# Kernel tuning notes

Hardware: AMD Instinct MI355X
Metric: run time of the kernel (lower is better)

The kernel has to match this reference:

```python
import jax, jax.numpy as jnp
import numpy as np

B, C, N = 2, 64, 40000
MLP = [64, 64, 128]
EPS = 1e-5


def setup_inputs() -> dict:
    key = jax.random.key(0)
    ks = jax.random.split(key, 2 + 4 * len(MLP))
    inp = {
        "points": jax.random.normal(ks[0], (B, C, N), dtype=jnp.float32),
        "near_idx": jax.random.randint(ks[1], (N, 6), 0, 2 * N, dtype=jnp.int32),
    }
    last = 2 * C
    for i, out_ch in enumerate(MLP):
        k = 2 + 4 * i
        scale = 1.0 / np.sqrt(last)
        inp[f"W{i}"] = jax.random.normal(ks[k], (out_ch, last), dtype=jnp.float32) * scale
        inp[f"b{i}"] = jax.random.normal(ks[k + 1], (out_ch,), dtype=jnp.float32) * 0.01
        inp[f"g{i}"] = jnp.ones((out_ch,), dtype=jnp.float32)
        inp[f"beta{i}"] = jnp.zeros((out_ch,), dtype=jnp.float32)
        last = out_ch
    return inp


def _mlp_bn_relu(x, W, b, g, beta):
    # x: [B, N, 6, Cin]; 1x1 conv == channel matmul
    y = jnp.einsum("bnkc,oc->bnko", x, W) + b
    mu = y.mean(axis=(0, 1, 2))
    var = y.var(axis=(0, 1, 2))  # biased, matches BN training normalization
    y = (y - mu) * jax.lax.rsqrt(var + EPS) * g + beta
    return jax.nn.relu(y)


def reference(points, near_idx, W0, b0, g0, beta0, W1, b1, g1, beta1, W2, b2, g2, beta2):
    x = jnp.transpose(points, (0, 2, 1))          # [B, N, C]
    pad = jnp.full_like(x, -1.0)                  # out-of-index block (-1 fill)
    xpad = jnp.concatenate([x, pad], axis=1)      # [B, 2N, C]
    near = xpad[:, near_idx, :]                   # [B, N, 6, C] irregular gather
    feat = jnp.concatenate(
        [jnp.broadcast_to(x[:, :, None, :], near.shape), near], axis=3
    )                                             # [B, N, 6, 2C]
    feat = _mlp_bn_relu(feat, W0, b0, g0, beta0)
    feat = _mlp_bn_relu(feat, W1, b1, g1, beta1)
    feat = _mlp_bn_relu(feat, W2, b2, g2, beta2)  # [B, N, 6, C']
    new_feature = feat.max(axis=2)                # max over 6 neighbors -> [B, N, C']
    new_feature = jnp.transpose(new_feature, (0, 2, 1))  # [B, C', N] (torch layout)
    out_feature = new_feature.max(axis=1)         # max over channels -> [B, N]
    return (out_feature, new_feature)
```

## Files before the change

kernel.cpp:

```cpp
#include <hip/hip_runtime.h>

typedef unsigned short u16;
typedef unsigned int uint;
typedef short bf16x8 __attribute__((ext_vector_type(8)));
typedef float f32x4 __attribute__((ext_vector_type(4)));

constexpr int B_ = 2;
constexpr int N_ = 40000;
constexpr int SPB = 240000;
constexpr int S_ = B_ * SPB;
constexpr float EPS_ = 1e-5f;
constexpr float INV_S = 1.0f / (float)S_;
constexpr int OF_ = B_ * N_;
constexpr int TILES_PB = SPB / 48;

constexpr int      WS_V_U16   = B_ * N_ * 128;
constexpr size_t   NEED_BIG_B = 81955072ull;

__device__ inline float b2f_lo(uint u) { return __builtin_bit_cast(float, u << 16); }
__device__ inline float b2f_hi(uint u) { return __builtin_bit_cast(float, u & 0xffff0000u); }
__device__ inline float b2fu(u16 s)    { return __builtin_bit_cast(float, ((uint)s) << 16); }
__device__ inline u16 f2b(float f) {
    uint b = __builtin_bit_cast(uint, f);
    return (u16)((b + 0x7fffu + ((b >> 16) & 1u)) >> 16);
}
__device__ inline uint pk2(float a, float b) { return (uint)f2b(a) | ((uint)f2b(b) << 16); }
__device__ inline void unp8(uint4 q, float* f) {
    f[0] = b2f_lo(q.x); f[1] = b2f_hi(q.x); f[2] = b2f_lo(q.y); f[3] = b2f_hi(q.y);
    f[4] = b2f_lo(q.z); f[5] = b2f_hi(q.z); f[6] = b2f_lo(q.w); f[7] = b2f_hi(q.w);
}

__global__ __launch_bounds__(256) void wprep_kernel(const float* __restrict__ W0,
                                                    const float* __restrict__ W1,
                                                    const float* __restrict__ W2,
                                                    float* __restrict__ stats,
                                                    float* __restrict__ neg2,
                                                    u16* __restrict__ pack) {
    const int t = threadIdx.x;
    stats[t] = 0.f; stats[t + 256] = 0.f;
    if (t < 64) {
        float s = 0.f;
        for (int j = 0; j < 64; ++j) s += W0[t * 128 + 64 + j];
        neg2[t] = -s;
    }
    for (int g = t; g < 40 * 64; g += 256) {
        int lane = g & 63, grp = g >> 6;
        int cb = lane & 15, kq = lane >> 4;
        ushort4 lo, hi;
        u16* dst;
        if (grp < 16) {
            int ct = grp >> 1, kk = grp & 1;
            int c = ct * 16 + cb, jb = kk * 32 + kq * 8;
            dst = pack + g * 8;
            float v[8];
            #pragma unroll
            for (int i = 0; i < 8; ++i)
                v[i] = (c < 64) ? W0[c * 128 + jb + i] : W0[(c - 64) * 128 + 64 + jb + i];
            lo = {f2b(v[0]), f2b(v[1]), f2b(v[2]), f2b(v[3])};
            hi = {f2b(v[4]), f2b(v[5]), f2b(v[6]), f2b(v[7])};
        } else if (grp < 24) {
            int g2 = grp - 16;
            int ct = g2 >> 1, kk = g2 & 1;
            const float* wp = W1 + (ct * 16 + cb) * 64 + kk * 32 + kq * 8;
            dst = pack + 8192 + (g2 * 64 + lane) * 8;
            lo = {f2b(wp[0]), f2b(wp[1]), f2b(wp[2]), f2b(wp[3])};
            hi = {f2b(wp[4]), f2b(wp[5]), f2b(wp[6]), f2b(wp[7])};
        } else {
            int g3 = grp - 24;
            int ct = g3 >> 1, kk = g3 & 1;
            const float* wp = W2 + (ct * 16 + cb) * 64 + kk * 32 + kq * 8;
            dst = pack + 12288 + (g3 * 64 + lane) * 8;
            lo = {f2b(wp[0]), f2b(wp[1]), f2b(wp[2]), f2b(wp[3])};
            hi = {f2b(wp[4]), f2b(wp[5]), f2b(wp[6]), f2b(wp[7])};
        }
        *(ushort4*)dst = lo;
        *(ushort4*)(dst + 4) = hi;
    }
}

__global__ __launch_bounds__(256) void p0_kernel(const float* __restrict__ pts,
                                                 const u16* __restrict__ pack,
                                                 u16* __restrict__ V) {
    const int t = threadIdx.x, lane = t & 63, w = t >> 6;
    const int cb = lane & 15, kq = lane >> 4;
    const int b = blockIdx.y;
    const int n0 = blockIdx.x * 192 + w * 48;
    const uint4* mp = (const uint4*)pack;

    bf16x8 af[3][2];
    #pragma unroll
    for (int mt = 0; mt < 3; ++mt) {
        int n = n0 + mt * 16 + cb;
        int nc = (n < N_) ? n : (N_ - 1);
        const float* xp = pts + b * 64 * N_ + nc;
        #pragma unroll
        for (int kk = 0; kk < 2; ++kk) {
            int jb = kk * 32 + kq * 8;
            #pragma unroll
            for (int i = 0; i < 8; ++i)
                af[mt][kk][i] = (short)f2b(xp[(size_t)(jb + i) * N_]);
        }
    }
    #pragma unroll
    for (int ct = 0; ct < 8; ++ct) {
        bf16x8 b0 = __builtin_bit_cast(bf16x8, mp[(ct * 2 + 0) * 64 + lane]);
        bf16x8 b1 = __builtin_bit_cast(bf16x8, mp[(ct * 2 + 1) * 64 + lane]);
        #pragma unroll
        for (int mt = 0; mt < 3; ++mt) {
            f32x4 acc = {};
            acc = __builtin_amdgcn_mfma_f32_16x16x32_bf16(af[mt][0], b0, acc, 0, 0, 0);
            acc = __builtin_amdgcn_mfma_f32_16x16x32_bf16(af[mt][1], b1, acc, 0, 0, 0);
            int rbase = n0 + mt * 16 + kq * 4;
            #pragma unroll
            for (int r = 0; r < 4; ++r) {
                int n = rbase + r;
                if (n < N_) V[(size_t)(b * N_ + n) * 128 + ct * 16 + cb] = f2b(acc[r]);
            }
        }
    }
}

__global__ __launch_bounds__(256) void p1_kernel(const u16* __restrict__ V,
                                                 const int* __restrict__ nidx,
                                                 const float* __restrict__ neg2,
                                                 float* __restrict__ stats) {
    const int t = threadIdx.x, lane = t & 63, w = t >> 6;
    const int slot = lane >> 3, cg = lane & 7;
    const int b = blockIdx.y;
    const int s0 = blockIdx.x * 384 + w * 96;
    float ngs8[8];
    #pragma unroll
    for (int i = 0; i < 8; ++i) ngs8[i] = neg2[cg * 8 + i];
    float sum[8] = {0,0,0,0,0,0,0,0}, sq[8] = {0,0,0,0,0,0,0,0};
    #pragma unroll
    for (int h = 0; h < 2; ++h) {
        int mh[6]; uint4 q1[6], q2[6]; bool val[6];
        #pragma unroll
        for (int it = 0; it < 6; ++it) {
            int s = s0 + (h * 6 + it) * 8 + slot;
            mh[it] = nidx[s];
            q1[it] = *(const uint4*)(V + (size_t)(b * N_ + s / 6) * 128 + cg * 8);
        }
        #pragma unroll
        for (int it = 0; it < 6; ++it) {
            val[it] = (mh[it] < N_);
            int row2 = val[it] ? (b * N_ + mh[it]) : 0;
            q2[it] = *(const uint4*)(V + (size_t)row2 * 128 + 64 + cg * 8);
        }
        #pragma unroll
        for (int it = 0; it < 6; ++it) {
            float v1[8], v2[8];
            unp8(q1[it], v1); unp8(q2[it], v2);
            #pragma unroll
            for (int i = 0; i < 8; ++i) {
                float z = v1[i] + (val[it] ? v2[i] : ngs8[i]);
                sum[i] += z; sq[i] = fmaf(z, z, sq[i]);
            }
        }
    }
    #pragma unroll
    for (int i = 0; i < 8; ++i) {
        sum[i] += __shfl_xor(sum[i], 8); sum[i] += __shfl_xor(sum[i], 16); sum[i] += __shfl_xor(sum[i], 32);
        sq[i]  += __shfl_xor(sq[i], 8);  sq[i]  += __shfl_xor(sq[i], 16);  sq[i]  += __shfl_xor(sq[i], 32);
    }
    __shared__ float red[2][4][64];
    if (slot == 0) {
        #pragma unroll
        for (int i = 0; i < 8; ++i) { red[0][w][cg * 8 + i] = sum[i]; red[1][w][cg * 8 + i] = sq[i]; }
    }
    __syncthreads();
    if (t < 64) {
        float s_ = (red[0][0][t] + red[0][1][t]) + (red[0][2][t] + red[0][3][t]);
        float q_ = (red[1][0][t] + red[1][1][t]) + (red[1][2][t] + red[1][3][t]);
        atomicAdd(&stats[t], s_);
        atomicAdd(&stats[64 + t], q_);
    }
}

__device__ inline bf16x8 build_af(const u16* __restrict__ V, int row1, int row2,
                                  const float* adt0, const float* adt1,
                                  const float* ngs, int j0) {
    float v1f[8], v2f[8];
    uint4 q1 = *(const uint4*)(V + (size_t)row1 * 128 + j0);
    unp8(q1, v1f);
    if (row2 >= 0) {
        uint4 q2 = *(const uint4*)(V + (size_t)row2 * 128 + 64 + j0);
        unp8(q2, v2f);
    } else {
        #pragma unroll
        for (int i = 0; i < 8; ++i) v2f[i] = ngs[j0 + i];
    }
    bf16x8 r;
    #pragma unroll
    for (int i = 0; i < 8; ++i) {
        float f0 = fmaxf((v1f[i] + v2f[i]) * adt0[j0 + i] + adt1[j0 + i], 0.f);
        r[i] = (short)f2b(f0);
    }
    return r;
}

__device__ inline int sigma_sl(int mt, int row) {
    int r_ = row & 3, kqr = row >> 2;
    int idx = mt * 4 + r_;
    int po = (idx >= 6) ? 1 : 0;
    return (kqr * 2 + po) * 6 + (idx - 6 * po);
}

template<int STOREZ1>
__global__ __launch_bounds__(256) void p2_kernel(const u16* __restrict__ V,
                                                 const int* __restrict__ nidx,
                                                 const float* __restrict__ neg2,
                                                 const u16* __restrict__ pack,
                                                 const float* __restrict__ g0,
                                                 const float* __restrict__ beta0,
                                                 float* __restrict__ stats,
                                                 u16* __restrict__ z1buf) {
    __shared__ float adt0[64], adt1[64], ngs[64];
    __shared__ float red[2][4][64];
    const int t = threadIdx.x, lane = t & 63, w = t >> 6;
    const int cb = lane & 15, kq = lane >> 4;
    if (t < 64) {
        float mu = stats[t] * INV_S, vr = stats[64 + t] * INV_S - mu * mu;
        float a = rsqrtf(vr + EPS_) * g0[t];
        adt0[t] = a; adt1[t] = beta0[t] - mu * a; ngs[t] = neg2[t];
    }
    __syncthreads();
    const int b = blockIdx.y;
    const int slb = blockIdx.x * 192 + w * 48;
    const uint4* w1p = (const uint4*)(pack + 8192);
    uint4* zt4 = STOREZ1 ? ((uint4*)z1buf + ((size_t)b * TILES_PB + blockIdx.x * 4 + w) * (6 * 64)) : nullptr;

    int m_[3];
    #pragma unroll
    for (int mt = 0; mt < 3; ++mt) m_[mt] = nidx[slb + sigma_sl(mt, cb)];

    bf16x8 bf[4][2];
    #pragma unroll
    for (int ct = 0; ct < 4; ++ct)
        #pragma unroll
        for (int kk = 0; kk < 2; ++kk)
            bf[ct][kk] = __builtin_bit_cast(bf16x8, w1p[(ct * 2 + kk) * 64 + lane]);

    float ssum[4] = {0,0,0,0}, ssq[4] = {0,0,0,0};
    #pragma unroll
    for (int mt = 0; mt < 3; ++mt) {
        int sl = slb + sigma_sl(mt, cb);
        int n = sl / 6;
        int row1 = b * N_ + n;
        int row2 = (m_[mt] < N_) ? (b * N_ + m_[mt]) : -1;
        bf16x8 af[2];
        #pragma unroll
        for (int kk = 0; kk < 2; ++kk)
            af[kk] = build_af(V, row1, row2, adt0, adt1, ngs, kk * 32 + kq * 8);
        f32x4 acc[4] = {};
        #pragma unroll
        for (int ct = 0; ct < 4; ++ct) {
            acc[ct] = __builtin_amdgcn_mfma_f32_16x16x32_bf16(af[0], bf[ct][0], acc[ct], 0, 0, 0);
            acc[ct] = __builtin_amdgcn_mfma_f32_16x16x32_bf16(af[1], bf[ct][1], acc[ct], 0, 0, 0);
        }
        #pragma unroll
        for (int ct = 0; ct < 4; ++ct)
            #pragma unroll
            for (int r = 0; r < 4; ++r) {
                float z = acc[ct][r];
                ssum[ct] += z; ssq[ct] = fmaf(z, z, ssq[ct]);
            }
        if constexpr (STOREZ1) {
            #pragma unroll
            for (int cp = 0; cp < 2; ++cp) {
                uint4 o;
                o.x = pk2(acc[cp * 2][0], acc[cp * 2][1]);
                o.y = pk2(acc[cp * 2][2], acc[cp * 2][3]);
                o.z = pk2(acc[cp * 2 + 1][0], acc[cp * 2 + 1][1]);
                o.w = pk2(acc[cp * 2 + 1][2], acc[cp * 2 + 1][3]);
                zt4[(mt * 2 + cp) * 64 + lane] = o;
            }
        }
    }
    #pragma unroll
    for (int ct = 0; ct < 4; ++ct) {
        ssum[ct] += __shfl_xor(ssum[ct], 16); ssum[ct] += __shfl_xor(ssum[ct], 32);
        ssq[ct]  += __shfl_xor(ssq[ct], 16);  ssq[ct]  += __shfl_xor(ssq[ct], 32);
    }
    if (lane < 16) {
        #pragma unroll
        for (int ct = 0; ct < 4; ++ct) {
            red[0][w][ct * 16 + lane] = ssum[ct];
            red[1][w][ct * 16 + lane] = ssq[ct];
        }
    }
    __syncthreads();
    if (t < 64) {
        float s = (red[0][0][t] + red[0][1][t]) + (red[0][2][t] + red[0][3][t]);
        float q = (red[1][0][t] + red[1][1][t]) + (red[1][2][t] + red[1][3][t]);
        atomicAdd(&stats[128 + t], s);
        atomicAdd(&stats[192 + t], q);
    }
}

__global__ __launch_bounds__(256) void p3big_kernel(const u16* __restrict__ z1buf,
                                                    const u16* __restrict__ pack,
                                                    const float* __restrict__ g1, const float* __restrict__ beta1,
                                                    const float* __restrict__ g2,
                                                    float* __restrict__ stats,
                                                    u16* __restrict__ raw) {
    __shared__ u16   f1t[4][2][1024];
    __shared__ float smax[32][129];
    __shared__ float red[2][4][128];
    __shared__ float adt2s[64], adt3s[64], psign[128];
    const int t = threadIdx.x, lane = t & 63, w = t >> 6;
    const int cb = lane & 15, kq = lane >> 4;
    if (t < 64) {
        float mu1 = stats[128 + t] * INV_S, vr1 = stats[192 + t] * INV_S - mu1 * mu1;
        float a1 = rsqrtf(vr1 + EPS_) * g1[t];
        adt2s[t] = a1; adt3s[t] = beta1[t] - mu1 * a1;
    }
    if (t < 128) psign[t] = (g2[t] >= 0.f) ? 1.f : -1.f;
    __syncthreads();

    const int b = blockIdx.y;
    const uint4* zt4 = (const uint4*)z1buf + ((size_t)b * TILES_PB + blockIdx.x * 4 + w) * (6 * 64);
    const uint4* w2p = (const uint4*)(pack + 12288);

    uint4 zq[6];
    #pragma unroll
    for (int i = 0; i < 6; ++i) zq[i] = zt4[i * 64 + lane];

    bf16x8 bf2[8][2];
    #pragma unroll
    for (int u = 0; u < 8; ++u)
        #pragma unroll
        for (int kk = 0; kk < 2; ++kk)
            bf2[u][kk] = __builtin_bit_cast(bf16x8, w2p[(u * 2 + kk) * 64 + lane]);

    float a1c[4], d1c[4];
    #pragma unroll
    for (int ct = 0; ct < 4; ++ct) { a1c[ct] = adt2s[ct * 16 + cb]; d1c[ct] = adt3s[ct * 16 + cb]; }

    float pmax_[2][4][2];
    #pragma unroll
    for (int h = 0; h < 2; ++h)
        #pragma unroll
        for (int ct = 0; ct < 4; ++ct) { pmax_[h][ct][0] = -3.402823466e+38f; pmax_[h][ct][1] = -3.402823466e+38f; }
    float ssum[8] = {0,0,0,0,0,0,0,0}, ssq[8] = {0,0,0,0,0,0,0,0};
    u16* fb0 = f1t[w][0];
    u16* fb1 = f1t[w][1];

    auto BNW = [&](int mt, u16* fb) {
        #pragma unroll
        for (int cp = 0; cp < 2; ++cp) {
            uint4 q = zq[mt * 2 + cp];
            float za[4] = {b2f_lo(q.x), b2f_hi(q.x), b2f_lo(q.y), b2f_hi(q.y)};
            float zb[4] = {b2f_lo(q.z), b2f_hi(q.z), b2f_lo(q.w), b2f_hi(q.w)};
            int ca = cp * 2, cc = cp * 2 + 1;
            #pragma unroll
            for (int r = 0; r < 4; ++r) {
                int rw = kq * 4 + r;
                fb[rw * 64 + ((ca * 16 + cb) ^ ((rw & 7) << 3))] = f2b(fmaxf(za[r] * a1c[ca] + d1c[ca], 0.f));
                fb[rw * 64 + ((cc * 16 + cb) ^ ((rw & 7) << 3))] = f2b(fmaxf(zb[r] * a1c[cc] + d1c[cc], 0.f));
            }
        }
    };
    auto RDA = [&](const u16* fb, bf16x8* af2) {
        #pragma unroll
        for (int kk = 0; kk < 2; ++kk) {
            int j0 = kk * 32 + kq * 8;
            af2[kk] = __builtin_bit_cast(bf16x8, *(const uint4*)(fb + cb * 64 + (j0 ^ ((cb & 7) << 3))));
        }
    };
    auto MM = [&](int mt, const bf16x8* af2) {
        #pragma unroll
        for (int half = 0; half < 2; ++half) {
            f32x4 acc2[4] = {};
            #pragma unroll
            for (int ct = 0; ct < 4; ++ct) {
                acc2[ct] = __builtin_amdgcn_mfma_f32_16x16x32_bf16(af2[0], bf2[half * 4 + ct][0], acc2[ct], 0, 0, 0);
                acc2[ct] = __builtin_amdgcn_mfma_f32_16x16x32_bf16(af2[1], bf2[half * 4 + ct][1], acc2[ct], 0, 0, 0);
            }
            #pragma unroll
            for (int ct = 0; ct < 4; ++ct) {
                float ps = psign[half * 64 + ct * 16 + cb];
                #pragma unroll
                for (int r = 0; r < 4; ++r) {
                    float z = acc2[ct][r];
                    ssum[half * 4 + ct] += z;
                    ssq[half * 4 + ct] = fmaf(z, z, ssq[half * 4 + ct]);
                    float zz = z * ps;
                    int pi = (mt == 0) ? 0 : ((mt == 2) ? 1 : ((r >= 2) ? 1 : 0));
                    pmax_[half][ct][pi] = fmaxf(pmax_[half][ct][pi], zz);
                }
            }
        }
    };

    bf16x8 afA[2], afB[2];
    BNW(0, fb0); BNW(1, fb1);
    RDA(fb0, afA);
    MM(0, afA);
    BNW(2, fb0);
    RDA(fb1, afB);
    MM(1, afB);
    RDA(fb0, afA);
    MM(2, afA);

    #pragma unroll
    for (int half = 0; half < 2; ++half)
        #pragma unroll
        for (int ct = 0; ct < 4; ++ct)
            #pragma unroll
            for (int p = 0; p < 2; ++p)
                smax[w * 8 + kq * 2 + p][half * 64 + ct * 16 + cb] = pmax_[half][ct][p];
    #pragma unroll
    for (int j = 0; j < 8; ++j) {
        ssum[j] += __shfl_xor(ssum[j], 16); ssum[j] += __shfl_xor(ssum[j], 32);
        ssq[j]  += __shfl_xor(ssq[j], 16);  ssq[j]  += __shfl_xor(ssq[j], 32);
    }
    if (lane < 16) {
        #pragma unroll
        for (int j = 0; j < 8; ++j) {
            int c = (j >> 2) * 64 + (j & 3) * 16 + lane;
            red[0][w][c] = ssum[j];
            red[1][w][c] = ssq[j];
        }
    }
    __syncthreads();
    if (t < 128) {
        float s = (red[0][0][t] + red[0][1][t]) + (red[0][2][t] + red[0][3][t]);
        float q = (red[1][0][t] + red[1][1][t]) + (red[1][2][t] + red[1][3][t]);
        atomicAdd(&stats[256 + t], s);
        atomicAdd(&stats[384 + t], q);
    }
    {
        int c2 = t >> 1, nh = t & 1;
        float ps = psign[c2];
        u16* rp = raw + ((size_t)b * 128 + c2) * N_ + blockIdx.x * 32 + nh * 16;
        #pragma unroll
        for (int i4 = 0; i4 < 4; ++i4) {
            ushort4 v;
            v.x = f2b(smax[nh * 16 + i4 * 4 + 0][c2] * ps);
            v.y = f2b(smax[nh * 16 + i4 * 4 + 1][c2] * ps);
            v.z = f2b(smax[nh * 16 + i4 * 4 + 2][c2] * ps);
            v.w = f2b(smax[nh * 16 + i4 * 4 + 3][c2] * ps);
            *(ushort4*)(rp + i4 * 4) = v;
        }
    }
}

__global__ __launch_bounds__(256) void p3small_kernel(const u16* __restrict__ V,
                                                      const int* __restrict__ nidx,
                                                      const float* __restrict__ neg2,
                                                      const u16* __restrict__ pack,
                                                      const float* __restrict__ g0, const float* __restrict__ beta0,
                                                      const float* __restrict__ g1, const float* __restrict__ beta1,
                                                      const float* __restrict__ g2,
                                                      float* __restrict__ stats,
                                                      float* __restrict__ out) {
    __shared__ u16   f1t[4][16 * 64];
    __shared__ float smax[32][129];
    __shared__ float red[2][4][128];
    __shared__ float adt2s[64], adt3s[64], psign[128];
    __shared__ float adt0s[64], adt1s[64], ngs[64];
    const int t = threadIdx.x, lane = t & 63, w = t >> 6;
    const int cb = lane & 15, kq = lane >> 4;
    if (t < 64) {
        float mu1 = stats[128 + t] * INV_S, vr1 = stats[192 + t] * INV_S - mu1 * mu1;
        float a1 = rsqrtf(vr1 + EPS_) * g1[t];
        adt2s[t] = a1; adt3s[t] = beta1[t] - mu1 * a1;
        float mu0 = stats[t] * INV_S, vr0 = stats[64 + t] * INV_S - mu0 * mu0;
        float a0 = rsqrtf(vr0 + EPS_) * g0[t];
        adt0s[t] = a0; adt1s[t] = beta0[t] - mu0 * a0; ngs[t] = neg2[t];
    }
    if (t < 128) psign[t] = (g2[t] >= 0.f) ? 1.f : -1.f;
    __syncthreads();

    const int b = blockIdx.y;
    const int slb = blockIdx.x * 192 + w * 48;
    const uint4* w1p = (const uint4*)(pack + 8192);
    const uint4* w2p = (const uint4*)(pack + 12288);

    bf16x8 bf2[8][2];
    #pragma unroll
    for (int u = 0; u < 8; ++u)
        #pragma unroll
        for (int kk = 0; kk < 2; ++kk)
            bf2[u][kk] = __builtin_bit_cast(bf16x8, w2p[(u * 2 + kk) * 64 + lane]);

    float a1c[4], d1c[4];
    #pragma unroll
    for (int ct = 0; ct < 4; ++ct) { a1c[ct] = adt2s[ct * 16 + cb]; d1c[ct] = adt3s[ct * 16 + cb]; }

    float pmax_[2][4][2];
    #pragma unroll
    for (int h = 0; h < 2; ++h)
        #pragma unroll
        for (int ct = 0; ct < 4; ++ct) { pmax_[h][ct][0] = -3.402823466e+38f; pmax_[h][ct][1] = -3.402823466e+38f; }
    float ssum[8] = {0,0,0,0,0,0,0,0}, ssq[8] = {0,0,0,0,0,0,0,0};
    u16* fb = f1t[w];

    #pragma unroll
    for (int mt = 0; mt < 3; ++mt) {
        bf16x8 bf1[4][2];
        #pragma unroll
        for (int ct = 0; ct < 4; ++ct)
            #pragma unroll
            for (int kk = 0; kk < 2; ++kk)
                bf1[ct][kk] = __builtin_bit_cast(bf16x8, w1p[(ct * 2 + kk) * 64 + lane]);
        int sl = slb + sigma_sl(mt, cb);
        int n = sl / 6;
        int m = nidx[sl];
        int row1 = b * N_ + n;
        int row2 = (m < N_) ? (b * N_ + m) : -1;
        bf16x8 af[2];
        #pragma unroll
        for (int kk = 0; kk < 2; ++kk)
            af[kk] = build_af(V, row1, row2, adt0s, adt1s, ngs, kk * 32 + kq * 8);
        f32x4 z1v[4];
        #pragma unroll
        for (int ct = 0; ct < 4; ++ct) {
            f32x4 a = {};
            a = __builtin_amdgcn_mfma_f32_16x16x32_bf16(af[0], bf1[ct][0], a, 0, 0, 0);
            a = __builtin_amdgcn_mfma_f32_16x16x32_bf16(af[1], bf1[ct][1], a, 0, 0, 0);
            z1v[ct] = a;
        }
        #pragma unroll
        for (int ct = 0; ct < 4; ++ct)
            #pragma unroll
            for (int r = 0; r < 4; ++r) {
                float f1 = fmaxf(z1v[ct][r] * a1c[ct] + d1c[ct], 0.f);
                int rw = kq * 4 + r;
                fb[rw * 64 + ((ct * 16 + cb) ^ ((rw & 7) << 3))] = f2b(f1);
            }
        bf16x8 af2[2];
        #pragma unroll
        for (int kk = 0; kk < 2; ++kk) {
            int j0 = kk * 32 + kq * 8;
            af2[kk] = __builtin_bit_cast(bf16x8, *(const uint4*)(fb + cb * 64 + (j0 ^ ((cb & 7) << 3))));
        }
        #pragma unroll
        for (int half = 0; half < 2; ++half) {
            f32x4 acc2[4] = {};
            #pragma unroll
            for (int ct = 0; ct < 4; ++ct) {
                acc2[ct] = __builtin_amdgcn_mfma_f32_16x16x32_bf16(af2[0], bf2[half * 4 + ct][0], acc2[ct], 0, 0, 0);
                acc2[ct] = __builtin_amdgcn_mfma_f32_16x16x32_bf16(af2[1], bf2[half * 4 + ct][1], acc2[ct], 0, 0, 0);
            }
            #pragma unroll
            for (int ct = 0; ct < 4; ++ct) {
                float ps = psign[half * 64 + ct * 16 + cb];
                #pragma unroll
                for (int r = 0; r < 4; ++r) {
                    float z = acc2[ct][r];
                    ssum[half * 4 + ct] += z;
                    ssq[half * 4 + ct] = fmaf(z, z, ssq[half * 4 + ct]);
                    float zz = z * ps;
                    int pi = (mt == 0) ? 0 : ((mt == 2) ? 1 : ((r >= 2) ? 1 : 0));
                    pmax_[half][ct][pi] = fmaxf(pmax_[half][ct][pi], zz);
                }
            }
        }
    }
    #pragma unroll
    for (int half = 0; half < 2; ++half)
        #pragma unroll
        for (int ct = 0; ct < 4; ++ct)
            #pragma unroll
            for (int p = 0; p < 2; ++p)
                smax[w * 8 + kq * 2 + p][half * 64 + ct * 16 + cb] = pmax_[half][ct][p];
    #pragma unroll
    for (int j = 0; j < 8; ++j) {
        ssum[j] += __shfl_xor(ssum[j], 16); ssum[j] += __shfl_xor(ssum[j], 32);
        ssq[j]  += __shfl_xor(ssq[j], 16);  ssq[j]  += __shfl_xor(ssq[j], 32);
    }
    if (lane < 16) {
        #pragma unroll
        for (int j = 0; j < 8; ++j) {
            int c = (j >> 2) * 64 + (j & 3) * 16 + lane;
            red[0][w][c] = ssum[j];
            red[1][w][c] = ssq[j];
        }
    }
    __syncthreads();
    if (t < 128) {
        float s = (red[0][0][t] + red[0][1][t]) + (red[0][2][t] + red[0][3][t]);
        float q = (red[1][0][t] + red[1][1][t]) + (red[1][2][t] + red[1][3][t]);
        atomicAdd(&stats[256 + t], s);
        atomicAdd(&stats[384 + t], q);
    }
    {
        int c2 = t >> 1, nh = t & 1;
        float ps = psign[c2];
        float* op = out + OF_ + ((size_t)b * 128 + c2) * N_ + blockIdx.x * 32 + nh * 16;
        #pragma unroll
        for (int i4 = 0; i4 < 4; ++i4) {
            float4 v;
            v.x = smax[nh * 16 + i4 * 4 + 0][c2] * ps;
            v.y = smax[nh * 16 + i4 * 4 + 1][c2] * ps;
            v.z = smax[nh * 16 + i4 * 4 + 2][c2] * ps;
            v.w = smax[nh * 16 + i4 * 4 + 3][c2] * ps;
            *(float4*)(op + i4 * 4) = v;
        }
    }
}

__global__ __launch_bounds__(256) void p4big_kernel(const float* __restrict__ g2,
                                                    const float* __restrict__ beta2,
                                                    const float* __restrict__ stats,
                                                    const u16* __restrict__ raw,
                                                    float* __restrict__ out) {
    __shared__ float a2s[128], d2s[128];
    __shared__ float vred[4][64];
    const int t = threadIdx.x, lane = t & 63, cg = t >> 6;
    if (t < 128) {
        float mu = stats[256 + t] * INV_S;
        float vr = stats[384 + t] * INV_S - mu * mu;
        float a = rsqrtf(vr + EPS_) * g2[t];
        a2s[t] = a;
        d2s[t] = beta2[t] - mu * a;
    }
    __syncthreads();
    const int b = blockIdx.y;
    const int n = blockIdx.x * 64 + lane;
    const u16* rp = raw + ((size_t)b * 128 + cg * 32) * N_ + n;
    float* op = out + OF_ + ((size_t)b * 128 + cg * 32) * N_ + n;
    float vmax = -3.402823466e+38f;
    #pragma unroll 8
    for (int c = 0; c < 32; ++c) {
        int c2 = cg * 32 + c;
        float v = fmaxf(b2fu(rp[(size_t)c * N_]) * a2s[c2] + d2s[c2], 0.f);
        op[(size_t)c * N_] = v;
        vmax = fmaxf(vmax, v);
    }
    vred[cg][lane] = vmax;
    __syncthreads();
    if (t < 64)
        out[b * N_ + blockIdx.x * 64 + t] =
            fmaxf(fmaxf(vred[0][t], vred[1][t]), fmaxf(vred[2][t], vred[3][t]));
}

__global__ __launch_bounds__(256) void p4small_kernel(const float* __restrict__ g2,
                                                      const float* __restrict__ beta2,
                                                      const float* __restrict__ stats,
                                                      float* __restrict__ outbuf) {
    __shared__ float a2s[128], d2s[128];
    const int t = threadIdx.x;
    if (t < 128) {
        float mu = stats[256 + t] * INV_S;
        float vr = stats[384 + t] * INV_S - mu * mu;
        float a = rsqrtf(vr + EPS_) * g2[t];
        a2s[t] = a;
        d2s[t] = beta2[t] - mu * a;
    }
    __syncthreads();
    const int b = blockIdx.y;
    const int n = blockIdx.x * 256 + t;
    if (n >= N_) return;
    float vmax = -3.402823466e+38f;
    #pragma unroll 8
    for (int c2 = 0; c2 < 128; ++c2) {
        size_t idx = OF_ + ((size_t)b * 128 + c2) * N_ + n;
        float v = fmaxf(outbuf[idx] * a2s[c2] + d2s[c2], 0.f);
        outbuf[idx] = v;
        vmax = fmaxf(vmax, v);
    }
    outbuf[b * N_ + n] = vmax;
}

extern "C" void kernel_launch(void* const* d_in, const int* in_sizes, int n_in,
                              void* d_out, int out_size, void* d_ws, size_t ws_size,
                              hipStream_t stream) {
    (void)in_sizes; (void)n_in; (void)out_size;
    const float* pts   = (const float*)d_in[0];
    const int*   nidx  = (const int*)d_in[1];
    const float* W0    = (const float*)d_in[2];
    const float* g0    = (const float*)d_in[4];
    const float* beta0 = (const float*)d_in[5];
    const float* W1    = (const float*)d_in[6];
    const float* g1    = (const float*)d_in[8];
    const float* beta1 = (const float*)d_in[9];
    const float* W2    = (const float*)d_in[10];
    const float* g2    = (const float*)d_in[12];
    const float* beta2 = (const float*)d_in[13];
    const bool big = ws_size >= NEED_BIG_B;
    u16*   V     = (u16*)d_ws;
    u16*   z1b   = big ? ((u16*)d_ws + WS_V_U16) : nullptr;
    float* stats = (float*)d_ws + (big ? 20480000 : 5120000);
    float* neg2  = stats + 512;
    u16*   pack  = (u16*)d_ws + (big ? 40961152 : 10241152);
    float* out   = (float*)d_out;

    hipLaunchKernelGGL(wprep_kernel, dim3(1), dim3(256), 0, stream, W0, W1, W2, stats, neg2, pack);
    hipLaunchKernelGGL(p0_kernel, dim3((N_ + 191) / 192, B_), dim3(256), 0, stream, pts, pack, V);
    hipLaunchKernelGGL(p1_kernel, dim3(SPB / 384, B_), dim3(256), 0, stream, V, nidx, neg2, stats);
    if (big) {
        hipLaunchKernelGGL((p2_kernel<1>), dim3(SPB / 192, B_), dim3(256), 0, stream,
                           V, nidx, neg2, pack, g0, beta0, stats, z1b);
        hipLaunchKernelGGL(p3big_kernel, dim3(TILES_PB / 4, B_), dim3(256), 0, stream,
                           z1b, pack, g1, beta1, g2, stats, V);
        hipLaunchKernelGGL(p4big_kernel, dim3(N_ / 64, B_), dim3(256), 0, stream,
                           g2, beta2, stats, V, out);
    } else {
        hipLaunchKernelGGL((p2_kernel<0>), dim3(SPB / 192, B_), dim3(256), 0, stream,
                           V, nidx, neg2, pack, g0, beta0, stats, nullptr);
        hipLaunchKernelGGL(p3small_kernel, dim3(SPB / 192, B_), dim3(256), 0, stream,
                           V, nidx, neg2, pack, g0, beta0, g1, beta1, g2, stats, out);
        hipLaunchKernelGGL(p4small_kernel, dim3((N_ + 255) / 256, B_), dim3(256), 0, stream,
                           g2, beta2, stats, out);
    }
}
```

Measured before the change: 298.5 us.

## Materialize layer-0 pre-activations in p1 and recompute layer-1 in p3 instead of storing z1

```diff
diff --git a/kernel.cpp b/kernel.cpp
--- a/kernel.cpp
+++ b/kernel.cpp
@@ -12,7 +12,6 @@
 constexpr float EPS_ = 1e-5f;
 constexpr float INV_S = 1.0f / (float)S_;
 constexpr int OF_ = B_ * N_;
-constexpr int TILES_PB = SPB / 48;
 
 constexpr int      WS_V_U16   = B_ * N_ * 128;
 constexpr size_t   NEED_BIG_B = 81955072ull;
@@ -120,14 +119,17 @@
     }
 }
 
+template<int STOREZ0>
 __global__ __launch_bounds__(256) void p1_kernel(const u16* __restrict__ V,
                                                  const int* __restrict__ nidx,
                                                  const float* __restrict__ neg2,
-                                                 float* __restrict__ stats) {
+                                                 float* __restrict__ stats,
+                                                 u16* __restrict__ z0) {
     const int t = threadIdx.x, lane = t & 63, w = t >> 6;
     const int slot = lane >> 3, cg = lane & 7;
     const int b = blockIdx.y;
     const int s0 = blockIdx.x * 384 + w * 96;
+    uint4* zw = STOREZ0 ? ((uint4*)z0 + (size_t)b * SPB * 8) : nullptr;
     float ngs8[8];
     #pragma unroll
     for (int i = 0; i < 8; ++i) ngs8[i] = neg2[cg * 8 + i];
@@ -149,12 +151,17 @@
         }
         #pragma unroll
         for (int it = 0; it < 6; ++it) {
-            float v1[8], v2[8];
+            float v1[8], v2[8], z[8];
             unp8(q1[it], v1); unp8(q2[it], v2);
             #pragma unroll
             for (int i = 0; i < 8; ++i) {
-                float z = v1[i] + (val[it] ? v2[i] : ngs8[i]);
-                sum[i] += z; sq[i] = fmaf(z, z, sq[i]);
+                z[i] = v1[i] + (val[it] ? v2[i] : ngs8[i]);
+                sum[i] += z[i]; sq[i] = fmaf(z[i], z[i], sq[i]);
+            }
+            if constexpr (STOREZ0) {
+                int s = s0 + (h * 6 + it) * 8 + slot;
+                uint4 o = {pk2(z[0], z[1]), pk2(z[2], z[3]), pk2(z[4], z[5]), pk2(z[6], z[7])};
+                zw[(size_t)s * 8 + cg] = o;
             }
         }
     }
@@ -199,6 +206,19 @@
     return r;
 }
 
+__device__ inline void af_from_z0(uint4 q1, uint4 q2, int kq,
+                                  const float* adt0, const float* adt1, bf16x8* af) {
+    float z1[8], z2[8];
+    unp8(q1, z1); unp8(q2, z2);
+    bf16x8 a0, a1;
+    #pragma unroll
+    for (int i = 0; i < 8; ++i) {
+        a0[i] = (short)f2b(fmaxf(z1[i] * adt0[kq * 8 + i] + adt1[kq * 8 + i], 0.f));
+        a1[i] = (short)f2b(fmaxf(z2[i] * adt0[32 + kq * 8 + i] + adt1[32 + kq * 8 + i], 0.f));
+    }
+    af[0] = a0; af[1] = a1;
+}
+
 __device__ inline int sigma_sl(int mt, int row) {
     int r_ = row & 3, kqr = row >> 2;
     int idx = mt * 4 + r_;
@@ -206,34 +226,33 @@
     return (kqr * 2 + po) * 6 + (idx - 6 * po);
 }
 
-template<int STOREZ1>
-__global__ __launch_bounds__(256) void p2_kernel(const u16* __restrict__ V,
-                                                 const int* __restrict__ nidx,
-                                                 const float* __restrict__ neg2,
-                                                 const u16* __restrict__ pack,
-                                                 const float* __restrict__ g0,
-                                                 const float* __restrict__ beta0,
-                                                 float* __restrict__ stats,
-                                                 u16* __restrict__ z1buf) {
-    __shared__ float adt0[64], adt1[64], ngs[64];
+__global__ __launch_bounds__(256) void p2big_kernel(const u16* __restrict__ z0,
+                                                    const u16* __restrict__ pack,
+                                                    const float* __restrict__ g0,
+                                                    const float* __restrict__ beta0,
+                                                    float* __restrict__ stats) {
+    __shared__ float adt0[64], adt1[64];
     __shared__ float red[2][4][64];
     const int t = threadIdx.x, lane = t & 63, w = t >> 6;
     const int cb = lane & 15, kq = lane >> 4;
     if (t < 64) {
         float mu = stats[t] * INV_S, vr = stats[64 + t] * INV_S - mu * mu;
         float a = rsqrtf(vr + EPS_) * g0[t];
-        adt0[t] = a; adt1[t] = beta0[t] - mu * a; ngs[t] = neg2[t];
+        adt0[t] = a; adt1[t] = beta0[t] - mu * a;
     }
     __syncthreads();
     const int b = blockIdx.y;
     const int slb = blockIdx.x * 192 + w * 48;
+    const uint4* zr = (const uint4*)z0 + (size_t)(b * SPB + slb) * 8;
     const uint4* w1p = (const uint4*)(pack + 8192);
-    uint4* zt4 = STOREZ1 ? ((uint4*)z1buf + ((size_t)b * TILES_PB + blockIdx.x * 4 + w) * (6 * 64)) : nullptr;
-
-    int m_[3];
-    #pragma unroll
-    for (int mt = 0; mt < 3; ++mt) m_[mt] = nidx[slb + sigma_sl(mt, cb)];
-
+
+    uint4 zq[6];
+    #pragma unroll
+    for (int mt = 0; mt < 3; ++mt) {
+        int sig = sigma_sl(mt, cb);
+        zq[mt * 2 + 0] = zr[sig * 8 + kq];
+        zq[mt * 2 + 1] = zr[sig * 8 + 4 + kq];
+    }
     bf16x8 bf[4][2];
     #pragma unroll
     for (int ct = 0; ct < 4; ++ct)
@@ -244,14 +263,8 @@
     float ssum[4] = {0,0,0,0}, ssq[4] = {0,0,0,0};
     #pragma unroll
     for (int mt = 0; mt < 3; ++mt) {
-        int sl = slb + sigma_sl(mt, cb);
-        int n = sl / 6;
-        int row1 = b * N_ + n;
-        int row2 = (m_[mt] < N_) ? (b * N_ + m_[mt]) : -1;
         bf16x8 af[2];
-        #pragma unroll
-        for (int kk = 0; kk < 2; ++kk)
-            af[kk] = build_af(V, row1, row2, adt0, adt1, ngs, kk * 32 + kq * 8);
+        af_from_z0(zq[mt * 2], zq[mt * 2 + 1], kq, adt0, adt1, af);
         f32x4 acc[4] = {};
         #pragma unroll
         for (int ct = 0; ct < 4; ++ct) {
@@ -265,17 +278,6 @@
                 float z = acc[ct][r];
                 ssum[ct] += z; ssq[ct] = fmaf(z, z, ssq[ct]);
             }
-        if constexpr (STOREZ1) {
-            #pragma unroll
-            for (int cp = 0; cp < 2; ++cp) {
-                uint4 o;
-                o.x = pk2(acc[cp * 2][0], acc[cp * 2][1]);
-                o.y = pk2(acc[cp * 2][2], acc[cp * 2][3]);
-                o.z = pk2(acc[cp * 2 + 1][0], acc[cp * 2 + 1][1]);
-                o.w = pk2(acc[cp * 2 + 1][2], acc[cp * 2 + 1][3]);
-                zt4[(mt * 2 + cp) * 64 + lane] = o;
-            }
-        }
     }
     #pragma unroll
     for (int ct = 0; ct < 4; ++ct) {
@@ -298,19 +300,23 @@
     }
 }
 
-__global__ __launch_bounds__(256) void p3big_kernel(const u16* __restrict__ z1buf,
+__global__ __launch_bounds__(256) void p3big_kernel(const u16* __restrict__ z0,
                                                     const u16* __restrict__ pack,
+                                                    const float* __restrict__ g0, const float* __restrict__ beta0,
                                                     const float* __restrict__ g1, const float* __restrict__ beta1,
                                                     const float* __restrict__ g2,
                                                     float* __restrict__ stats,
                                                     u16* __restrict__ raw) {
-    __shared__ u16   f1t[4][2][1024];
+    __shared__ u16   f1t[4][1024];
     __shared__ float smax[32][129];
     __shared__ float red[2][4][128];
-    __shared__ float adt2s[64], adt3s[64], psign[128];
+    __shared__ float adt0s[64], adt1s[64], adt2s[64], adt3s[64], psign[128];
     const int t = threadIdx.x, lane = t & 63, w = t >> 6;
     const int cb = lane & 15, kq = lane >> 4;
     if (t < 64) {
+        float mu0 = stats[t] * INV_S, vr0 = stats[64 + t] * INV_S - mu0 * mu0;
+        float a0 = rsqrtf(vr0 + EPS_) * g0[t];
+        adt0s[t] = a0; adt1s[t] = beta0[t] - mu0 * a0;
         float mu1 = stats[128 + t] * INV_S, vr1 = stats[192 + t] * INV_S - mu1 * mu1;
         float a1 = rsqrtf(vr1 + EPS_) * g1[t];
         adt2s[t] = a1; adt3s[t] = beta1[t] - mu1 * a1;
@@ -319,13 +325,18 @@
     __syncthreads();
 
     const int b = blockIdx.y;
-    const uint4* zt4 = (const uint4*)z1buf + ((size_t)b * TILES_PB + blockIdx.x * 4 + w) * (6 * 64);
+    const int slb = blockIdx.x * 192 + w * 48;
+    const uint4* zr = (const uint4*)z0 + (size_t)(b * SPB + slb) * 8;
+    const uint4* w1p = (const uint4*)(pack + 8192);
     const uint4* w2p = (const uint4*)(pack + 12288);
 
     uint4 zq[6];
     #pragma unroll
-    for (int i = 0; i < 6; ++i) zq[i] = zt4[i * 64 + lane];
-
+    for (int mt = 0; mt < 3; ++mt) {
+        int sig = sigma_sl(mt, cb);
+        zq[mt * 2 + 0] = zr[sig * 8 + kq];
+        zq[mt * 2 + 1] = zr[sig * 8 + 4 + kq];
+    }
     bf16x8 bf2[8][2];
     #pragma unroll
     for (int u = 0; u < 8; ++u)
@@ -343,32 +354,40 @@
         #pragma unroll
         for (int ct = 0; ct < 4; ++ct) { pmax_[h][ct][0] = -3.402823466e+38f; pmax_[h][ct][1] = -3.402823466e+38f; }
     float ssum[8] = {0,0,0,0,0,0,0,0}, ssq[8] = {0,0,0,0,0,0,0,0};
-    u16* fb0 = f1t[w][0];
-    u16* fb1 = f1t[w][1];
-
-    auto BNW = [&](int mt, u16* fb) {
-        #pragma unroll
-        for (int cp = 0; cp < 2; ++cp) {
-            uint4 q = zq[mt * 2 + cp];
-            float za[4] = {b2f_lo(q.x), b2f_hi(q.x), b2f_lo(q.y), b2f_hi(q.y)};
-            float zb[4] = {b2f_lo(q.z), b2f_hi(q.z), b2f_lo(q.w), b2f_hi(q.w)};
-            int ca = cp * 2, cc = cp * 2 + 1;
+    u16* fb = f1t[w];
+
+    #pragma unroll
+    for (int mt = 0; mt < 3; ++mt) {
+        bf16x8 af[2];
+        af_from_z0(zq[mt * 2], zq[mt * 2 + 1], kq, adt0s, adt1s, af);
+        bf16x8 bf1[4][2];
+        #pragma unroll
+        for (int ct = 0; ct < 4; ++ct)
+            #pragma unroll
+            for (int kk = 0; kk < 2; ++kk)
+                bf1[ct][kk] = __builtin_bit_cast(bf16x8, w1p[(ct * 2 + kk) * 64 + lane]);
+        f32x4 z1v[4];
+        #pragma unroll
+        for (int ct = 0; ct < 4; ++ct) {
+            f32x4 a = {};
+            a = __builtin_amdgcn_mfma_f32_16x16x32_bf16(af[0], bf1[ct][0], a, 0, 0, 0);
+            a = __builtin_amdgcn_mfma_f32_16x16x32_bf16(af[1], bf1[ct][1], a, 0, 0, 0);
+            z1v[ct] = a;
+        }
+        #pragma unroll
+        for (int ct = 0; ct < 4; ++ct)
             #pragma unroll
             for (int r = 0; r < 4; ++r) {
+                float f1 = fmaxf(z1v[ct][r] * a1c[ct] + d1c[ct], 0.f);
                 int rw = kq * 4 + r;
-                fb[rw * 64 + ((ca * 16 + cb) ^ ((rw & 7) << 3))] = f2b(fmaxf(za[r] * a1c[ca] + d1c[ca], 0.f));
-                fb[rw * 64 + ((cc * 16 + cb) ^ ((rw & 7) << 3))] = f2b(fmaxf(zb[r] * a1c[cc] + d1c[cc], 0.f));
-            }
-        }
-    };
-    auto RDA = [&](const u16* fb, bf16x8* af2) {
+                fb[rw * 64 + ((ct * 16 + cb) ^ ((rw & 7) << 3))] = f2b(f1);
+            }
+        bf16x8 af2[2];
         #pragma unroll
         for (int kk = 0; kk < 2; ++kk) {
             int j0 = kk * 32 + kq * 8;
             af2[kk] = __builtin_bit_cast(bf16x8, *(const uint4*)(fb + cb * 64 + (j0 ^ ((cb & 7) << 3))));
         }
-    };
-    auto MM = [&](int mt, const bf16x8* af2) {
         #pragma unroll
         for (int half = 0; half < 2; ++half) {
             f32x4 acc2[4] = {};
@@ -391,18 +410,7 @@
                 }
             }
         }
-    };
-
-    bf16x8 afA[2], afB[2];
-    BNW(0, fb0); BNW(1, fb1);
-    RDA(fb0, afA);
-    MM(0, afA);
-    BNW(2, fb0);
-    RDA(fb1, afB);
-    MM(1, afB);
-    RDA(fb0, afA);
-    MM(2, afA);
-
+    }
     #pragma unroll
     for (int half = 0; half < 2; ++half)
         #pragma unroll
@@ -443,6 +451,79 @@
             v.w = f2b(smax[nh * 16 + i4 * 4 + 3][c2] * ps);
             *(ushort4*)(rp + i4 * 4) = v;
         }
+    }
+}
+
+__global__ __launch_bounds__(256) void p2small_kernel(const u16* __restrict__ V,
+                                                      const int* __restrict__ nidx,
+                                                      const float* __restrict__ neg2,
+                                                      const u16* __restrict__ pack,
+                                                      const float* __restrict__ g0,
+                                                      const float* __restrict__ beta0,
+                                                      float* __restrict__ stats) {
+    __shared__ float adt0[64], adt1[64], ngs[64];
+    __shared__ float red[2][4][64];
+    const int t = threadIdx.x, lane = t & 63, w = t >> 6;
+    const int cb = lane & 15, kq = lane >> 4;
+    if (t < 64) {
+        float mu = stats[t] * INV_S, vr = stats[64 + t] * INV_S - mu * mu;
+        float a = rsqrtf(vr + EPS_) * g0[t];
+        adt0[t] = a; adt1[t] = beta0[t] - mu * a; ngs[t] = neg2[t];
+    }
+    __syncthreads();
+    const int b = blockIdx.y;
+    const int slb = blockIdx.x * 192 + w * 48;
+    const uint4* w1p = (const uint4*)(pack + 8192);
+    bf16x8 bf[4][2];
+    #pragma unroll
+    for (int ct = 0; ct < 4; ++ct)
+        #pragma unroll
+        for (int kk = 0; kk < 2; ++kk)
+            bf[ct][kk] = __builtin_bit_cast(bf16x8, w1p[(ct * 2 + kk) * 64 + lane]);
+    float ssum[4] = {0,0,0,0}, ssq[4] = {0,0,0,0};
+    #pragma unroll
+    for (int mt = 0; mt < 3; ++mt) {
+        int sl = slb + sigma_sl(mt, cb);
+        int n = sl / 6;
+        int m = nidx[sl];
+        int row1 = b * N_ + n;
+        int row2 = (m < N_) ? (b * N_ + m) : -1;
+        bf16x8 af[2];
+        #pragma unroll
+        for (int kk = 0; kk < 2; ++kk)
+            af[kk] = build_af(V, row1, row2, adt0, adt1, ngs, kk * 32 + kq * 8);
+        f32x4 acc[4] = {};
+        #pragma unroll
+        for (int ct = 0; ct < 4; ++ct) {
+            acc[ct] = __builtin_amdgcn_mfma_f32_16x16x32_bf16(af[0], bf[ct][0], acc[ct], 0, 0, 0);
+            acc[ct] = __builtin_amdgcn_mfma_f32_16x16x32_bf16(af[1], bf[ct][1], acc[ct], 0, 0, 0);
+        }
+        #pragma unroll
+        for (int ct = 0; ct < 4; ++ct)
+            #pragma unroll
+            for (int r = 0; r < 4; ++r) {
+                float z = acc[ct][r];
+                ssum[ct] += z; ssq[ct] = fmaf(z, z, ssq[ct]);
+            }
+    }
+    #pragma unroll
+    for (int ct = 0; ct < 4; ++ct) {
+        ssum[ct] += __shfl_xor(ssum[ct], 16); ssum[ct] += __shfl_xor(ssum[ct], 32);
+        ssq[ct]  += __shfl_xor(ssq[ct], 16);  ssq[ct]  += __shfl_xor(ssq[ct], 32);
+    }
+    if (lane < 16) {
+        #pragma unroll
+        for (int ct = 0; ct < 4; ++ct) {
+            red[0][w][ct * 16 + lane] = ssum[ct];
+            red[1][w][ct * 16 + lane] = ssq[ct];
+        }
+    }
+    __syncthreads();
+    if (t < 64) {
+        float s = (red[0][0][t] + red[0][1][t]) + (red[0][2][t] + red[0][3][t]);
+        float q = (red[1][0][t] + red[1][1][t]) + (red[1][2][t] + red[1][3][t]);
+        atomicAdd(&stats[128 + t], s);
+        atomicAdd(&stats[192 + t], q);
     }
 }
 
@@ -455,7 +536,7 @@
                                                       const float* __restrict__ g2,
                                                       float* __restrict__ stats,
                                                       float* __restrict__ out) {
-    __shared__ u16   f1t[4][16 * 64];
+    __shared__ u16   f1t[4][1024];
     __shared__ float smax[32][129];
     __shared__ float red[2][4][128];
     __shared__ float adt2s[64], adt3s[64], psign[128];
@@ -472,23 +553,19 @@
     }
     if (t < 128) psign[t] = (g2[t] >= 0.f) ? 1.f : -1.f;
     __syncthreads();
-
     const int b = blockIdx.y;
     const int slb = blockIdx.x * 192 + w * 48;
     const uint4* w1p = (const uint4*)(pack + 8192);
     const uint4* w2p = (const uint4*)(pack + 12288);
-
     bf16x8 bf2[8][2];
     #pragma unroll
     for (int u = 0; u < 8; ++u)
         #pragma unroll
         for (int kk = 0; kk < 2; ++kk)
             bf2[u][kk] = __builtin_bit_cast(bf16x8, w2p[(u * 2 + kk) * 64 + lane]);
-
     float a1c[4], d1c[4];
     #pragma unroll
     for (int ct = 0; ct < 4; ++ct) { a1c[ct] = adt2s[ct * 16 + cb]; d1c[ct] = adt3s[ct * 16 + cb]; }
-
     float pmax_[2][4][2];
     #pragma unroll
     for (int h = 0; h < 2; ++h)
@@ -496,7 +573,6 @@
         for (int ct = 0; ct < 4; ++ct) { pmax_[h][ct][0] = -3.402823466e+38f; pmax_[h][ct][1] = -3.402823466e+38f; }
     float ssum[8] = {0,0,0,0,0,0,0,0}, ssq[8] = {0,0,0,0,0,0,0,0};
     u16* fb = f1t[w];
-
     #pragma unroll
     for (int mt = 0; mt < 3; ++mt) {
         bf16x8 bf1[4][2];
@@ -682,7 +758,7 @@
     const float* beta2 = (const float*)d_in[13];
     const bool big = ws_size >= NEED_BIG_B;
     u16*   V     = (u16*)d_ws;
-    u16*   z1b   = big ? ((u16*)d_ws + WS_V_U16) : nullptr;
+    u16*   z0b   = big ? ((u16*)d_ws + WS_V_U16) : nullptr;
     float* stats = (float*)d_ws + (big ? 20480000 : 5120000);
     float* neg2  = stats + 512;
     u16*   pack  = (u16*)d_ws + (big ? 40961152 : 10241152);
@@ -690,17 +766,16 @@
 
     hipLaunchKernelGGL(wprep_kernel, dim3(1), dim3(256), 0, stream, W0, W1, W2, stats, neg2, pack);
     hipLaunchKernelGGL(p0_kernel, dim3((N_ + 191) / 192, B_), dim3(256), 0, stream, pts, pack, V);
-    hipLaunchKernelGGL(p1_kernel, dim3(SPB / 384, B_), dim3(256), 0, stream, V, nidx, neg2, stats);
     if (big) {
-        hipLaunchKernelGGL((p2_kernel<1>), dim3(SPB / 192, B_), dim3(256), 0, stream,
-                           V, nidx, neg2, pack, g0, beta0, stats, z1b);
-        hipLaunchKernelGGL(p3big_kernel, dim3(TILES_PB / 4, B_), dim3(256), 0, stream,
-                           z1b, pack, g1, beta1, g2, stats, V);
-        hipLaunchKernelGGL(p4big_kernel, dim3(N_ / 64, B_), dim3(256), 0, stream,
-                           g2, beta2, stats, V, out);
+        hipLaunchKernelGGL((p1_kernel<1>), dim3(SPB / 384, B_), dim3(256), 0, stream, V, nidx, neg2, stats, z0b);
+        hipLaunchKernelGGL(p2big_kernel, dim3(SPB / 192, B_), dim3(256), 0, stream, z0b, pack, g0, beta0, stats);
+        hipLaunchKernelGGL(p3big_kernel, dim3(SPB / 192, B_), dim3(256), 0, stream,
+                           z0b, pack, g0, beta0, g1, beta1, g2, stats, V);
+        hipLaunchKernelGGL(p4big_kernel, dim3(N_ / 64, B_), dim3(256), 0, stream, g2, beta2, stats, V, out);
     } else {
-        hipLaunchKernelGGL((p2_kernel<0>), dim3(SPB / 192, B_), dim3(256), 0, stream,
-                           V, nidx, neg2, pack, g0, beta0, stats, nullptr);
+        hipLaunchKernelGGL((p1_kernel<0>), dim3(SPB / 384, B_), dim3(256), 0, stream, V, nidx, neg2, stats, nullptr);
+        hipLaunchKernelGGL(p2small_kernel, dim3(SPB / 192, B_), dim3(256), 0, stream,
+                           V, nidx, neg2, pack, g0, beta0, stats);
         hipLaunchKernelGGL(p3small_kernel, dim3(SPB / 192, B_), dim3(256), 0, stream,
                            V, nidx, neg2, pack, g0, beta0, g1, beta1, g2, stats, out);
         hipLaunchKernelGGL(p4small_kernel, dim3((N_ + 255) / 256, B_), dim3(256), 0, stream,
```

Measured after the change: 304.1 us. No clear change (+1.9%).
